# Kernel optimization log

Measured on AMD Instinct MI355X. Metric: run time of the kernel, lower is better.

## Reference

```python
import jax, jax.numpy as jnp
import numpy as np

B, S, HID, NH = 2, 2048, 2048, 16
ROPE, NOPE, VDIM = 64, 64, 128
QHEAD = ROPE + NOPE            # 128
QLORA = HID // 3               # 682
KVLORA = HID // 8              # 256
THETA = 128000.0
SCALE = 1.0 / np.sqrt(QHEAD)   # deepseek softmax_scale = q_head_dim**-0.5
EPS = 1e-6


def rmsnorm(x, w):
    var = jnp.mean(x.astype(jnp.float32) ** 2, axis=-1, keepdims=True)
    return (x.astype(jnp.float32) * jax.lax.rsqrt(var + EPS)).astype(x.dtype) * w


def rope_cos_sin(seq, dim, theta):
    inv = 1.0 / (theta ** (jnp.arange(0, dim, 2, dtype=jnp.float32) / dim))
    t = jnp.arange(seq, dtype=jnp.float32)
    freqs = jnp.outer(t, inv)                      # [S, dim/2]
    emb = jnp.concatenate([freqs, freqs], axis=-1)  # [S, dim]
    return jnp.cos(emb), jnp.sin(emb)


def apply_rope(x, cos, sin):
    # deepseek interleave: view(b,h,s,d/2,2).transpose(-1,-2).reshape, then rotate_half rope
    b, h, s, d = x.shape
    x = x.reshape(b, h, s, d // 2, 2).transpose(0, 1, 2, 4, 3).reshape(b, h, s, d)
    x1, x2 = jnp.split(x, 2, axis=-1)
    rot = jnp.concatenate([-x2, x1], axis=-1)
    return x * cos + rot * sin


def setup_inputs() -> dict:
    key = jax.random.key(0)
    ks = jax.random.split(key, 8)
    s = lambda fan_in: 1.0 / np.sqrt(fan_in)
    return {
        "x":        jax.random.normal(ks[0], (B, S, HID), jnp.float32),
        "q_a_w":    jax.random.normal(ks[1], (HID, QLORA), jnp.float32) * s(HID),
        "q_a_ln_w": jnp.ones((QLORA,), jnp.float32),
        "q_b_w":    jax.random.normal(ks[2], (QLORA, NH * QHEAD), jnp.float32) * s(QLORA),
        "kv_a_w":   jax.random.normal(ks[3], (HID, KVLORA + ROPE), jnp.float32) * s(HID),
        "kv_a_ln_w": jnp.ones((KVLORA,), jnp.float32),
        "kv_b_w":   jax.random.normal(ks[4], (KVLORA, NH * (NOPE + VDIM)), jnp.float32) * s(KVLORA),
        "o_w":      jax.random.normal(ks[5], (NH * VDIM, HID), jnp.float32) * s(NH * VDIM),
    }


def reference(x, q_a_w, q_a_ln_w, q_b_w, kv_a_w, kv_a_ln_w, kv_b_w, o_w):
    b, s, _ = x.shape
    # Q: low-rank down-proj -> RMSNorm -> up-proj
    q = rmsnorm(x @ q_a_w, q_a_ln_w) @ q_b_w               # [b,s,NH*QHEAD]
    q = q.reshape(b, s, NH, QHEAD).transpose(0, 2, 1, 3)   # [b,NH,s,QHEAD]
    q_nope, q_pe = q[..., :NOPE], q[..., NOPE:]
    # KV: compressed latent + shared rope key
    ckv_kpe = x @ kv_a_w                                   # [b,s,KVLORA+ROPE]
    ckv, k_pe = ckv_kpe[..., :KVLORA], ckv_kpe[..., KVLORA:]
    k_pe = k_pe.reshape(b, 1, s, ROPE)                     # shared across heads
    kv = rmsnorm(ckv, kv_a_ln_w) @ kv_b_w                  # [b,s,NH*(NOPE+VDIM)]
    kv = kv.reshape(b, s, NH, NOPE + VDIM).transpose(0, 2, 1, 3)
    k_nope, v = kv[..., :NOPE], kv[..., NOPE:]             # [b,NH,s,NOPE], [b,NH,s,VDIM]
    # decoupled RoPE on the rope split only
    cos, sin = rope_cos_sin(s, ROPE, THETA)
    q_pe = apply_rope(q_pe, cos, sin)
    k_pe = apply_rope(k_pe, cos, sin)
    qf = jnp.concatenate([q_nope, q_pe], axis=-1)          # [b,NH,s,QHEAD]
    kf = jnp.concatenate([k_nope, jnp.broadcast_to(k_pe, (b, NH, s, ROPE))], axis=-1)
    scores = jnp.einsum('bhqd,bhkd->bhqk', qf, kf) * SCALE
    causal = jnp.tril(jnp.ones((s, s), bool))
    scores = jnp.where(causal, scores, jnp.float32(-1e9))
    attn = jax.nn.softmax(scores.astype(jnp.float32), axis=-1).astype(qf.dtype)
    out = jnp.einsum('bhqk,bhkd->bhqd', attn, v)           # [b,NH,s,VDIM]
    out = out.transpose(0, 2, 1, 3).reshape(b, s, NH * VDIM)
    return out @ o_w                                       # [b,s,HID]
```

## Files before the change

kernel.cpp:

```cpp
#include <hip/hip_runtime.h>
#include <hip/hip_bf16.h>

typedef __attribute__((ext_vector_type(8))) short short8;
typedef __attribute__((ext_vector_type(4))) float f32x4;

using bf16 = __hip_bfloat16;

static constexpr int B_ = 2, S_ = 2048, HID_ = 2048, NH_ = 16;
static constexpr int ROPE_ = 64, VDIM_ = 128, QHEAD_ = 128;
static constexpr int QLORA_ = 682, KVLORA_ = 256;
static constexpr int QLORA_P = 704;
static constexpr int NQA_P = 768;
static constexpr int NKVA_P = 384;
static constexpr int NA_ = NQA_P + NKVA_P;
static constexpr float THETA_ = 128000.0f;
static constexpr float SCALE_ = 0.08838834764831845f;
static constexpr float SCL2_ = 0.08838834764831845f * 1.4426950408889634f;
static constexpr float EPS_ = 1e-6f;
static constexpr int BS_ = B_ * S_;

__device__ __forceinline__ void gl2lds16(const void* g, void* l) {
    __builtin_amdgcn_global_load_lds(
        (const __attribute__((address_space(1))) unsigned int*)g,
        (__attribute__((address_space(3))) unsigned int*)l, 16, 0, 0);
}

struct bf16x4_s { bf16 x, y, z, w; };

struct TD { const float* src; bf16* dst; int Ksrc, Nsrc, Kpad, tilesX, off, perm; };
struct TDs { TD d[5]; };
static constexpr int PREP_TILES = 8576;

__global__ void k_prep(TDs P, const float* __restrict__ x, bf16* __restrict__ xb,
                       float* __restrict__ ct, float* __restrict__ st) {
    __shared__ float tile[32][33];
    if (blockIdx.x >= PREP_TILES) {
        int bid = blockIdx.x - PREP_TILES;
        int t = threadIdx.y * 32 + threadIdx.x;
        if (bid < 8192) {
            int i = bid * 256 + t;
            float4 v = reinterpret_cast<const float4*>(x)[i];
            bf16x4_s o;
            o.x = __float2bfloat16(v.x); o.y = __float2bfloat16(v.y);
            o.z = __float2bfloat16(v.z); o.w = __float2bfloat16(v.w);
            reinterpret_cast<bf16x4_s*>(xb)[i] = o;
        } else {
            int idx = (bid - 8192) * 256 + t;
            int tpos = idx >> 5, j = idx & 31;
            float inv = expf(-(float)j * (logf(THETA_) / 32.0f));
            float f = (float)tpos * inv;
            ct[idx] = cosf(f);
            st[idx] = sinf(f);
        }
        return;
    }
    int flat = blockIdx.x;
    int di = 0;
    #pragma unroll
    for (int i = 1; i < 5; ++i) if (flat >= P.d[i].off) di = i;
    TD d = P.d[di];
    int local = flat - d.off;
    int xt = local % d.tilesX, yt = local / d.tilesX;
    int kb = xt * 32, nb = yt * 32;
    int tx = threadIdx.x, ty = threadIdx.y;
    #pragma unroll
    for (int i = 0; i < 32; i += 8) {
        int k = kb + ty + i, n = nb + tx;
        tile[ty + i][tx] = (k < d.Ksrc && n < d.Nsrc) ? d.src[(size_t)k * d.Nsrc + n] : 0.0f;
    }
    __syncthreads();
    #pragma unroll
    for (int i = 0; i < 32; i += 8) {
        int n = nb + ty + i, k = kb + tx;
        int nd = n;
        if (d.perm) {
            int h = n / 192, dd = n - h * 192;
            nd = (dd < 64) ? h * 64 + dd : 1024 + h * 128 + (dd - 64);
        }
        d.dst[(size_t)nd * d.Kpad + k] = __float2bfloat16(tile[tx][ty + i]);
    }
}

#define GEMM_PROLOGUE(Aptr, Bptr, LDA, LDB, KDIM)                                        \
    __shared__ bf16 As[128 * 64];                                                        \
    __shared__ bf16 Bs[128 * 64];                                                        \
    const int t = threadIdx.x;                                                           \
    const int lane = t & 63, w = t >> 6;                                                 \
    const int l15 = lane & 15, l4 = lane >> 4;                                           \
    const int wr = (w >> 1) * 64, wc = (w & 1) * 64;                                     \
    const int m0 = blockIdx.y * 128, n0 = blockIdx.x * 128;                              \
    f32x4 acc[4][4] = {};                                                                \
    for (int k0 = 0; k0 < (KDIM); k0 += 64) {                                            \
        _Pragma("unroll")                                                                \
        for (int i = 0; i < 4; ++i) {                                                    \
            int cid = t + i * 256;                                                       \
            int row = cid >> 3;                                                          \
            int ch = (cid & 7) ^ (row & 7);                                              \
            gl2lds16((Aptr) + (size_t)(m0 + row) * (LDA) + k0 + ch * 8,                  \
                     reinterpret_cast<char*>(As) + cid * 16);                            \
            gl2lds16((Bptr) + (size_t)(n0 + row) * (LDB) + k0 + ch * 8,                  \
                     reinterpret_cast<char*>(Bs) + cid * 16);                            \
        }                                                                                \
        __syncthreads();                                                                 \
        _Pragma("unroll")                                                                \
        for (int kk = 0; kk < 2; ++kk) {                                                 \
            short8 a[4], b[4];                                                           \
            _Pragma("unroll")                                                            \
            for (int m = 0; m < 4; ++m) {                                                \
                int row = wr + m * 16 + l15;                                             \
                int ch = (kk * 4 + l4) ^ (row & 7);                                      \
                a[m] = *reinterpret_cast<const short8*>(                                 \
                    reinterpret_cast<const char*>(As) + row * 128 + ch * 16);            \
            }                                                                            \
            _Pragma("unroll")                                                            \
            for (int n = 0; n < 4; ++n) {                                                \
                int row = wc + n * 16 + l15;                                             \
                int ch = (kk * 4 + l4) ^ (row & 7);                                      \
                b[n] = *reinterpret_cast<const short8*>(                                 \
                    reinterpret_cast<const char*>(Bs) + row * 128 + ch * 16);            \
            }                                                                            \
            _Pragma("unroll")                                                            \
            for (int m = 0; m < 4; ++m)                                                  \
                _Pragma("unroll")                                                        \
                for (int n = 0; n < 4; ++n)                                              \
                    acc[m][n] = __builtin_amdgcn_mfma_f32_16x16x32_bf16(a[m], b[n],      \
                                                                       acc[m][n], 0, 0, 0); \
        }                                                                                \
        __syncthreads();                                                                 \
    }

template <typename OutT>
__launch_bounds__(256)
__global__ void gemm_bt(const bf16* __restrict__ A, const bf16* __restrict__ Bt,
                        OutT* __restrict__ C, int K, int lda, int ldb, int ldc)
{
    GEMM_PROLOGUE(A, Bt, lda, ldb, K)
    #pragma unroll
    for (int m = 0; m < 4; ++m)
        #pragma unroll
        for (int n = 0; n < 4; ++n)
            #pragma unroll
            for (int j = 0; j < 4; ++j) {
                int r = m0 + wr + m * 16 + l4 * 4 + j;
                int c = n0 + wc + n * 16 + l15;
                float v = acc[m][n][j];
                if constexpr (sizeof(OutT) == 2) C[(size_t)r * ldc + c] = __float2bfloat16(v);
                else                             C[(size_t)r * ldc + c] = v;
            }
}

__launch_bounds__(256)
__global__ void gemm_qb_rope(const bf16* __restrict__ A, const bf16* __restrict__ Bt,
                             const float* __restrict__ ct, const float* __restrict__ st,
                             bf16* __restrict__ Qf)
{
    GEMM_PROLOGUE(A, Bt, QLORA_P, QLORA_P, QLORA_P)
    const int h = blockIdx.x;
    if (wc == 0) {
        #pragma unroll
        for (int m = 0; m < 4; ++m)
            #pragma unroll
            for (int n = 0; n < 4; ++n)
                #pragma unroll
                for (int j = 0; j < 4; ++j) {
                    int r = m0 + wr + m * 16 + l4 * 4 + j;
                    int c = n * 16 + l15;
                    int s = r & (S_ - 1), bq = r >> 11;
                    Qf[((size_t)(bq * NH_ + h) * S_ + s) * 128 + c] =
                        __float2bfloat16(acc[m][n][j] * SCL2_);
                }
    } else {
        #pragma unroll
        for (int m = 0; m < 4; ++m)
            #pragma unroll
            for (int n = 0; n < 4; ++n)
                #pragma unroll
                for (int j = 0; j < 4; ++j) {
                    int r = m0 + wr + m * 16 + l4 * 4 + j;
                    int p = n * 16 + l15;
                    int jj = p >> 1, odd = p & 1;
                    float v = acc[m][n][j];
                    float pr = __shfl_xor(v, 1);
                    float e0 = odd ? pr : v, e1 = odd ? v : pr;
                    int s = r & (S_ - 1), bq = r >> 11;
                    float c_ = ct[s * 32 + jj], s_ = st[s * 32 + jj];
                    float ov = odd ? (e1 * c_ + e0 * s_) : (e0 * c_ - e1 * s_);
                    int c_out = 64 + (odd ? 32 : 0) + jj;
                    Qf[((size_t)(bq * NH_ + h) * S_ + s) * 128 + c_out] =
                        __float2bfloat16(ov * SCL2_);
                }
    }
}

__launch_bounds__(256)
__global__ void gemm_kvb_split(const bf16* __restrict__ A, const bf16* __restrict__ Bt,
                               bf16* __restrict__ knope, bf16* __restrict__ Vt)
{
    GEMM_PROLOGUE(A, Bt, KVLORA_, KVLORA_, KVLORA_)
    if (n0 < 1024) {
        #pragma unroll
        for (int m = 0; m < 4; ++m)
            #pragma unroll
            for (int n = 0; n < 4; ++n)
                #pragma unroll
                for (int j = 0; j < 4; ++j) {
                    int r = m0 + wr + m * 16 + l4 * 4 + j;
                    int c = n0 + wc + n * 16 + l15;
                    knope[(size_t)r * 1024 + c] = __float2bfloat16(acc[m][n][j]);
                }
    } else {
        const int h = (n0 - 1024) >> 7;
        const int bq = m0 >> 11;
        const int bh = bq * NH_ + h;
        #pragma unroll
        for (int m = 0; m < 4; ++m)
            #pragma unroll
            for (int n = 0; n < 4; ++n) {
                int cl = wc + n * 16 + l15;
                int rb = m0 + wr + m * 16 + l4 * 4;
                int s = rb & (S_ - 1);
                ushort4 pk;
                {
                    bf16 h0 = __float2bfloat16(acc[m][n][0]);
                    bf16 h1 = __float2bfloat16(acc[m][n][1]);
                    bf16 h2 = __float2bfloat16(acc[m][n][2]);
                    bf16 h3 = __float2bfloat16(acc[m][n][3]);
                    pk.x = *reinterpret_cast<unsigned short*>(&h0);
                    pk.y = *reinterpret_cast<unsigned short*>(&h1);
                    pk.z = *reinterpret_cast<unsigned short*>(&h2);
                    pk.w = *reinterpret_cast<unsigned short*>(&h3);
                }
                *reinterpret_cast<ushort4*>(Vt + ((size_t)bh * 128 + cl) * S_ + s) = pk;
            }
    }
}

__launch_bounds__(256)
__global__ void k_rms_rope(const bf16* __restrict__ qac,
                           const float* __restrict__ qln, const float* __restrict__ kvln,
                           const float* __restrict__ ct, const float* __restrict__ st,
                           bf16* __restrict__ qan, bf16* __restrict__ ckvn, bf16* __restrict__ kr)
{
    __shared__ float red[8];
    int bs = blockIdx.x;
    int t = threadIdx.x, lane = t & 63, w = t >> 6;
    int s = bs & (S_ - 1);
    const bf16* qrow = qac + (size_t)bs * NA_;
    const bf16* crow = qrow + NQA_P;
    float sq = 0.f, sk;
    for (int c = t; c < QLORA_; c += 256) { float v = __bfloat162float(qrow[c]); sq += v * v; }
    { float v = __bfloat162float(crow[t]); sk = v * v; }
    #pragma unroll
    for (int m = 1; m < 64; m <<= 1) { sq += __shfl_xor(sq, m); sk += __shfl_xor(sk, m); }
    if (lane == 0) { red[w] = sq; red[4 + w] = sk; }
    __syncthreads();
    sq = red[0] + red[1] + red[2] + red[3];
    sk = red[4] + red[5] + red[6] + red[7];
    float qs = rsqrtf(sq / (float)QLORA_ + EPS_);
    float ks = rsqrtf(sk / (float)KVLORA_ + EPS_);
    for (int c = t; c < QLORA_P; c += 256)
        qan[(size_t)bs * QLORA_P + c] =
            (c < QLORA_) ? __float2bfloat16(__bfloat162float(qrow[c]) * qs * qln[c])
                         : __float2bfloat16(0.0f);
    ckvn[(size_t)bs * KVLORA_ + t] = __float2bfloat16(__bfloat162float(crow[t]) * ks * kvln[t]);
    if (t < 64) {
        int j = t & 31;
        float c_ = ct[s * 32 + j], s_ = st[s * 32 + j];
        float e0 = __bfloat162float(crow[KVLORA_ + 2 * j]);
        float e1 = __bfloat162float(crow[KVLORA_ + 2 * j + 1]);
        float v = (t < 32) ? (e0 * c_ - e1 * s_) : (e1 * c_ + e0 * s_);
        kr[(size_t)bs * 64 + t] = __float2bfloat16(v);
    }
}

__launch_bounds__(512, 4)
__global__ void k_flash(const bf16* __restrict__ Qf, const bf16* __restrict__ knope,
                        const bf16* __restrict__ kr, const bf16* __restrict__ Vt,
                        bf16* __restrict__ attn_out)
{
    __shared__ bf16 Ks[2][64 * 128];
    __shared__ bf16 Vs[2][128 * 64];
    __shared__ bf16 Ps[8][16 * 64];

    const int t = threadIdx.x, lane = t & 63, w = t >> 6;
    const int l15 = lane & 15, l4 = lane >> 4;
    const int qb = (blockIdx.y < 8) ? (15 - blockIdx.y) : (blockIdx.y - 8);
    const int bh = blockIdx.x;
    const int q0 = qb * 128;
    const int b = bh >> 4, h = bh & 15;
    const int r0 = q0 + w * 16;

    short8 qa_[4];
    {
        const bf16* qrow = Qf + ((size_t)bh * S_ + r0 + l15) * 128;
        #pragma unroll
        for (int kk = 0; kk < 4; ++kk)
            qa_[kk] = *reinterpret_cast<const short8*>(qrow + kk * 32 + l4 * 8);
    }

    const bf16 *kSrc0, *kSrc1, *vSrc0, *vSrc1;
    size_t kStp0, kStp1;
    {
        int cid = t, row = cid >> 4, ch = (cid & 15) ^ (row & 7);
        kSrc0 = (ch < 8) ? knope + (size_t)(b * S_ + row) * 1024 + h * 64 + ch * 8
                         : kr + (size_t)(b * S_ + row) * 64 + (ch - 8) * 8;
        kStp0 = (ch < 8) ? (size_t)64 * 1024 : (size_t)64 * 64;
    }
    {
        int cid = t + 512, row = cid >> 4, ch = (cid & 15) ^ (row & 7);
        kSrc1 = (ch < 8) ? knope + (size_t)(b * S_ + row) * 1024 + h * 64 + ch * 8
                         : kr + (size_t)(b * S_ + row) * 64 + (ch - 8) * 8;
        kStp1 = (ch < 8) ? (size_t)64 * 1024 : (size_t)64 * 64;
    }
    {
        const bf16* Vg = Vt + (size_t)bh * 128 * S_;
        int cid = t, row = cid >> 3, ch = (cid & 7) ^ (row & 7);
        vSrc0 = Vg + (size_t)row * S_ + ch * 8;
        cid = t + 512; row = cid >> 3; ch = (cid & 7) ^ (row & 7);
        vSrc1 = Vg + (size_t)row * S_ + ch * 8;
    }
    auto stage = [&](int buf) {
        gl2lds16(kSrc0, reinterpret_cast<char*>(Ks[buf]) + t * 16);
        gl2lds16(kSrc1, reinterpret_cast<char*>(Ks[buf]) + (t + 512) * 16);
        gl2lds16(vSrc0, reinterpret_cast<char*>(Vs[buf]) + t * 16);
        gl2lds16(vSrc1, reinterpret_cast<char*>(Vs[buf]) + (t + 512) * 16);
        kSrc0 += kStp0; kSrc1 += kStp1; vSrc0 += 64; vSrc1 += 64;
    };

    const int NT = qb * 2 + 2;
    stage(0);
    __syncthreads();

    f32x4 o[8] = {};
    float m_r[4], l_r[4];
    #pragma unroll
    for (int j = 0; j < 4; ++j) { m_r[j] = -1e30f; l_r[j] = 0.f; }

    int cur = 0;
    for (int kb = 0; kb < NT; ++kb) {
        const int k0 = kb * 64;
        if (kb + 1 < NT) stage(cur ^ 1);

        if (k0 <= r0 + 15) {
            f32x4 sfr[4] = {};
            __builtin_amdgcn_s_setprio(1);
            #pragma unroll
            for (int kk = 0; kk < 4; ++kk) {
                short8 bfr[4];
                #pragma unroll
                for (int n = 0; n < 4; ++n) {
                    int row = n * 16 + l15;
                    int ch = (kk * 4 + l4) ^ (row & 7);
                    bfr[n] = *reinterpret_cast<const short8*>(
                        reinterpret_cast<const char*>(Ks[cur]) + row * 256 + ch * 16);
                }
                #pragma unroll
                for (int n = 0; n < 4; ++n)
                    sfr[n] = __builtin_amdgcn_mfma_f32_16x16x32_bf16(qa_[kk], bfr[n], sfr[n], 0, 0, 0);
            }
            __builtin_amdgcn_s_setprio(0);

            const bool needMask = (k0 + 63 > r0);
            if (needMask) {
                #pragma unroll
                for (int n = 0; n < 4; ++n)
                    #pragma unroll
                    for (int j = 0; j < 4; ++j) {
                        int col = k0 + n * 16 + l15;
                        int row = r0 + l4 * 4 + j;
                        if (col > row) sfr[n][j] = -1e30f;
                    }
            }

            float rm[4];
            bool grow = false;
            #pragma unroll
            for (int j = 0; j < 4; ++j) {
                float r = fmaxf(fmaxf(sfr[0][j], sfr[1][j]), fmaxf(sfr[2][j], sfr[3][j]));
                r = fmaxf(r, __shfl_xor(r, 1));
                r = fmaxf(r, __shfl_xor(r, 2));
                r = fmaxf(r, __shfl_xor(r, 4));
                r = fmaxf(r, __shfl_xor(r, 8));
                rm[j] = r;
                grow |= (r > m_r[j] + 8.0f);
            }
            if (__ballot(grow)) {
                #pragma unroll
                for (int j = 0; j < 4; ++j) {
                    float mn = fmaxf(m_r[j], rm[j]);
                    float alpha = exp2f(m_r[j] - mn);
                    m_r[j] = mn;
                    l_r[j] *= alpha;
                    #pragma unroll
                    for (int n = 0; n < 8; ++n) o[n][j] *= alpha;
                }
            }

            char* pb = reinterpret_cast<char*>(Ps[w]);
            #pragma unroll
            for (int j = 0; j < 4; ++j) {
                float rs = 0.f;
                #pragma unroll
                for (int n = 0; n < 4; ++n) {
                    float p = exp2f(sfr[n][j] - m_r[j]);
                    sfr[n][j] = p;
                    rs += p;
                }
                rs += __shfl_xor(rs, 1); rs += __shfl_xor(rs, 2);
                rs += __shfl_xor(rs, 4); rs += __shfl_xor(rs, 8);
                l_r[j] += rs;
                int row = l4 * 4 + j;
                #pragma unroll
                for (int n = 0; n < 4; ++n) {
                    int col = n * 16 + l15;
                    int ch = (col >> 3) ^ (row & 7);
                    *reinterpret_cast<bf16*>(pb + row * 128 + ch * 16 + (col & 7) * 2) =
                        __float2bfloat16(sfr[n][j]);
                }
            }
            __builtin_amdgcn_s_setprio(1);
            #pragma unroll
            for (int kk = 0; kk < 2; ++kk) {
                int pch = (kk * 4 + l4) ^ (l15 & 7);
                short8 pa = *reinterpret_cast<const short8*>(pb + l15 * 128 + pch * 16);
                #pragma unroll
                for (int n = 0; n < 8; ++n) {
                    int row = n * 16 + l15;
                    int ch = (kk * 4 + l4) ^ (row & 7);
                    short8 vb = *reinterpret_cast<const short8*>(
                        reinterpret_cast<const char*>(Vs[cur]) + row * 128 + ch * 16);
                    o[n] = __builtin_amdgcn_mfma_f32_16x16x32_bf16(pa, vb, o[n], 0, 0, 0);
                }
            }
            __builtin_amdgcn_s_setprio(0);
        }
        __syncthreads();
        cur ^= 1;
    }

    size_t obase = ((size_t)(b * S_) + q0 + w * 16) * (size_t)(NH_ * VDIM_) + h * VDIM_;
    #pragma unroll
    for (int n = 0; n < 8; ++n)
        #pragma unroll
        for (int j = 0; j < 4; ++j) {
            int r = l4 * 4 + j;
            int c = n * 16 + l15;
            attn_out[obase + (size_t)r * (NH_ * VDIM_) + c] = __float2bfloat16(o[n][j] / l_r[j]);
        }
}

extern "C" void kernel_launch(void* const* d_in, const int* in_sizes, int n_in,
                              void* d_out, int out_size, void* d_ws, size_t ws_size,
                              hipStream_t stream)
{
    (void)in_sizes; (void)n_in; (void)out_size;
    const float* x       = (const float*)d_in[0];
    const float* q_a_w   = (const float*)d_in[1];
    const float* q_a_ln  = (const float*)d_in[2];
    const float* q_b_w   = (const float*)d_in[3];
    const float* kv_a_w  = (const float*)d_in[4];
    const float* kv_a_ln = (const float*)d_in[5];
    const float* kv_b_w  = (const float*)d_in[6];
    const float* o_w     = (const float*)d_in[7];
    float* out = (float*)d_out;

    char* ws = (char*)d_ws;
    size_t off = 0;
    auto alloc = [&](size_t bytes) -> char* {
        char* p = ws + off;
        off += (bytes + 255) & ~(size_t)255;
        return p;
    };

    bf16* xb     = (bf16*)alloc((size_t)BS_ * HID_ * 2);
    bf16* a_wt   = (bf16*)alloc((size_t)NA_ * HID_ * 2);
    bf16* qb_wt  = (bf16*)alloc((size_t)2048 * QLORA_P * 2);
    bf16* kvb_wt = (bf16*)alloc((size_t)3072 * KVLORA_ * 2);
    bf16* ow_t   = (bf16*)alloc((size_t)2048 * 2048 * 2);
    float* ct    = (float*)alloc((size_t)S_ * 32 * 4);
    float* st    = (float*)alloc((size_t)S_ * 32 * 4);
    bf16* qac    = (bf16*)alloc((size_t)BS_ * NA_ * 2);
    bf16* qan    = (bf16*)alloc((size_t)BS_ * QLORA_P * 2);
    bf16* ckvn   = (bf16*)alloc((size_t)BS_ * KVLORA_ * 2);
    bf16* kr     = (bf16*)alloc((size_t)BS_ * 64 * 2);
    bf16* knope  = (bf16*)alloc((size_t)BS_ * 1024 * 2);
    bf16* Vt     = (bf16*)alloc((size_t)BS_ * 2048 * 2);
    bf16* attn   = (bf16*)alloc((size_t)BS_ * 2048 * 2);

    bf16* Qf = xb;

    if (ws_size < off) return;

    TDs P;
    P.d[0] = TD{ q_a_w,  a_wt,                      2048,  682, 2048, 64,    0, 0 };
    P.d[1] = TD{ kv_a_w, a_wt + (size_t)NQA_P*2048, 2048,  320, 2048, 64, 1536, 0 };
    P.d[2] = TD{ q_b_w,  qb_wt,                      682, 2048,  704, 22, 2304, 0 };
    P.d[3] = TD{ kv_b_w, kvb_wt,                     256, 3072,  256,  8, 3712, 1 };
    P.d[4] = TD{ o_w,    ow_t,                      2048, 2048, 2048, 64, 4480, 0 };
    k_prep<<<PREP_TILES + 8192 + 256, dim3(32, 8), 0, stream>>>(P, x, xb, ct, st);

    gemm_bt<bf16><<<dim3(NA_ / 128, BS_ / 128), 256, 0, stream>>>(xb, a_wt, qac,
                                                                  HID_, HID_, HID_, NA_);

    k_rms_rope<<<BS_, 256, 0, stream>>>(qac, q_a_ln, kv_a_ln, ct, st, qan, ckvn, kr);

    gemm_qb_rope<<<dim3(2048 / 128, BS_ / 128), 256, 0, stream>>>(qan, qb_wt, ct, st, Qf);
    gemm_kvb_split<<<dim3(3072 / 128, BS_ / 128), 256, 0, stream>>>(ckvn, kvb_wt, knope, Vt);

    k_flash<<<dim3(B_ * NH_, S_ / 128), 512, 0, stream>>>(Qf, knope, kr, Vt, attn);

    gemm_bt<float><<<dim3(2048 / 128, BS_ / 128), 256, 0, stream>>>(attn, ow_t, out,
                                                                    HID_, HID_, HID_, 2048);
}
```

Baseline: 264.8 us.

## Merge Q/KV up-projection GEMMs into one launch and transpose flash S tile

Fuses the q_b+rope GEMM and the kv_b split GEMM into a single kernel whose grid is partitioned by blockIdx.x, removing a launch and letting both GEMMs share the device at once. In the flash kernel the QK^T MFMA operands are swapped so each lane holds scores for a single query row. This turns per-row max/sum reductions into two cross-lane shuffles instead of four per row for four rows, and lets P be written as packed bf16x4 stores. Rescale factors are now broadcast by shuffle, which adds some shuffle work on rescale and at the final normalization.

```diff
diff --git a/kernel.cpp b/kernel.cpp
--- a/kernel.cpp
+++ b/kernel.cpp
@@ -81,14 +81,16 @@
     }
 }
 
-#define GEMM_PROLOGUE(Aptr, Bptr, LDA, LDB, KDIM)                                        \
+#define GEMM_VARS                                                                        \
     __shared__ bf16 As[128 * 64];                                                        \
     __shared__ bf16 Bs[128 * 64];                                                        \
     const int t = threadIdx.x;                                                           \
     const int lane = t & 63, w = t >> 6;                                                 \
     const int l15 = lane & 15, l4 = lane >> 4;                                           \
-    const int wr = (w >> 1) * 64, wc = (w & 1) * 64;                                     \
-    const int m0 = blockIdx.y * 128, n0 = blockIdx.x * 128;                              \
+    const int wr = (w >> 1) * 64, wc = (w & 1) * 64;
+
+#define GEMM_CORE(Aptr, Bptr, LDA, LDB, KDIM, M0V, N0V)                                  \
+    const int m0 = (M0V), n0 = (N0V);                                                    \
     f32x4 acc[4][4] = {};                                                                \
     for (int k0 = 0; k0 < (KDIM); k0 += 64) {                                            \
         _Pragma("unroll")                                                                \
@@ -134,7 +136,8 @@
 __global__ void gemm_bt(const bf16* __restrict__ A, const bf16* __restrict__ Bt,
                         OutT* __restrict__ C, int K, int lda, int ldb, int ldc)
 {
-    GEMM_PROLOGUE(A, Bt, lda, ldb, K)
+    GEMM_VARS
+    GEMM_CORE(A, Bt, lda, ldb, K, blockIdx.y * 128, blockIdx.x * 128)
     #pragma unroll
     for (int m = 0; m < 4; ++m)
         #pragma unroll
@@ -150,88 +153,90 @@
 }
 
 __launch_bounds__(256)
-__global__ void gemm_qb_rope(const bf16* __restrict__ A, const bf16* __restrict__ Bt,
-                             const float* __restrict__ ct, const float* __restrict__ st,
-                             bf16* __restrict__ Qf)
+__global__ void gemm_up(const bf16* __restrict__ qan, const bf16* __restrict__ qb_wt,
+                        const float* __restrict__ ct, const float* __restrict__ st,
+                        bf16* __restrict__ Qf,
+                        const bf16* __restrict__ ckvn, const bf16* __restrict__ kvb_wt,
+                        bf16* __restrict__ knope, bf16* __restrict__ Vt)
 {
-    GEMM_PROLOGUE(A, Bt, QLORA_P, QLORA_P, QLORA_P)
-    const int h = blockIdx.x;
-    if (wc == 0) {
-        #pragma unroll
-        for (int m = 0; m < 4; ++m)
-            #pragma unroll
-            for (int n = 0; n < 4; ++n)
-                #pragma unroll
-                for (int j = 0; j < 4; ++j) {
-                    int r = m0 + wr + m * 16 + l4 * 4 + j;
-                    int c = n * 16 + l15;
-                    int s = r & (S_ - 1), bq = r >> 11;
-                    Qf[((size_t)(bq * NH_ + h) * S_ + s) * 128 + c] =
-                        __float2bfloat16(acc[m][n][j] * SCL2_);
+    GEMM_VARS
+    if (blockIdx.x < 16) {
+        GEMM_CORE(qan, qb_wt, QLORA_P, QLORA_P, QLORA_P, blockIdx.y * 128, blockIdx.x * 128)
+        (void)n0;
+        const int h = blockIdx.x;
+        if (wc == 0) {
+            #pragma unroll
+            for (int m = 0; m < 4; ++m)
+                #pragma unroll
+                for (int n = 0; n < 4; ++n)
+                    #pragma unroll
+                    for (int j = 0; j < 4; ++j) {
+                        int r = m0 + wr + m * 16 + l4 * 4 + j;
+                        int c = n * 16 + l15;
+                        int s = r & (S_ - 1), bq = r >> 11;
+                        Qf[((size_t)(bq * NH_ + h) * S_ + s) * 128 + c] =
+                            __float2bfloat16(acc[m][n][j] * SCL2_);
+                    }
+        } else {
+            #pragma unroll
+            for (int m = 0; m < 4; ++m)
+                #pragma unroll
+                for (int n = 0; n < 4; ++n)
+                    #pragma unroll
+                    for (int j = 0; j < 4; ++j) {
+                        int r = m0 + wr + m * 16 + l4 * 4 + j;
+                        int p = n * 16 + l15;
+                        int jj = p >> 1, odd = p & 1;
+                        float v = acc[m][n][j];
+                        float pr = __shfl_xor(v, 1);
+                        float e0 = odd ? pr : v, e1 = odd ? v : pr;
+                        int s = r & (S_ - 1), bq = r >> 11;
+                        float c_ = ct[s * 32 + jj], s_ = st[s * 32 + jj];
+                        float ov = odd ? (e1 * c_ + e0 * s_) : (e0 * c_ - e1 * s_);
+                        int c_out = 64 + (odd ? 32 : 0) + jj;
+                        Qf[((size_t)(bq * NH_ + h) * S_ + s) * 128 + c_out] =
+                            __float2bfloat16(ov * SCL2_);
+                    }
+        }
+    } else {
+        GEMM_CORE(ckvn, kvb_wt, KVLORA_, KVLORA_, KVLORA_, blockIdx.y * 128,
+                  (blockIdx.x - 16) * 128)
+        if (n0 < 1024) {
+            #pragma unroll
+            for (int m = 0; m < 4; ++m)
+                #pragma unroll
+                for (int n = 0; n < 4; ++n)
+                    #pragma unroll
+                    for (int j = 0; j < 4; ++j) {
+                        int r = m0 + wr + m * 16 + l4 * 4 + j;
+                        int c = n0 + wc + n * 16 + l15;
+                        knope[(size_t)r * 1024 + c] = __float2bfloat16(acc[m][n][j]);
+                    }
+        } else {
+            const int h = (n0 - 1024) >> 7;
+            const int bq = m0 >> 11;
+            const int bh = bq * NH_ + h;
+            #pragma unroll
+            for (int m = 0; m < 4; ++m)
+                #pragma unroll
+                for (int n = 0; n < 4; ++n) {
+                    int cl = wc + n * 16 + l15;
+                    int rb = m0 + wr + m * 16 + l4 * 4;
+                    int s = rb & (S_ - 1);
+                    ushort4 pk;
+                    {
+                        bf16 h0 = __float2bfloat16(acc[m][n][0]);
+                        bf16 h1 = __float2bfloat16(acc[m][n][1]);
+                        bf16 h2 = __float2bfloat16(acc[m][n][2]);
+                        bf16 h3 = __float2bfloat16(acc[m][n][3]);
+                        pk.x = *reinterpret_cast<unsigned short*>(&h0);
+                        pk.y = *reinterpret_cast<unsigned short*>(&h1);
+                        pk.z = *reinterpret_cast<unsigned short*>(&h2);
+                        pk.w = *reinterpret_cast<unsigned short*>(&h3);
+                    }
+                    *reinterpret_cast<ushort4*>(Vt + ((size_t)bh * 128 + cl) * S_ + s) = pk;
                 }
-    } else {
-        #pragma unroll
-        for (int m = 0; m < 4; ++m)
-            #pragma unroll
-            for (int n = 0; n < 4; ++n)
-                #pragma unroll
-                for (int j = 0; j < 4; ++j) {
-                    int r = m0 + wr + m * 16 + l4 * 4 + j;
-                    int p = n * 16 + l15;
-                    int jj = p >> 1, odd = p & 1;
-                    float v = acc[m][n][j];
-                    float pr = __shfl_xor(v, 1);
-                    float e0 = odd ? pr : v, e1 = odd ? v : pr;
-                    int s = r & (S_ - 1), bq = r >> 11;
-                    float c_ = ct[s * 32 + jj], s_ = st[s * 32 + jj];
-                    float ov = odd ? (e1 * c_ + e0 * s_) : (e0 * c_ - e1 * s_);
-                    int c_out = 64 + (odd ? 32 : 0) + jj;
-                    Qf[((size_t)(bq * NH_ + h) * S_ + s) * 128 + c_out] =
-                        __float2bfloat16(ov * SCL2_);
-                }
-    }
-}
-
-__launch_bounds__(256)
-__global__ void gemm_kvb_split(const bf16* __restrict__ A, const bf16* __restrict__ Bt,
-                               bf16* __restrict__ knope, bf16* __restrict__ Vt)
-{
-    GEMM_PROLOGUE(A, Bt, KVLORA_, KVLORA_, KVLORA_)
-    if (n0 < 1024) {
-        #pragma unroll
-        for (int m = 0; m < 4; ++m)
-            #pragma unroll
-            for (int n = 0; n < 4; ++n)
-                #pragma unroll
-                for (int j = 0; j < 4; ++j) {
-                    int r = m0 + wr + m * 16 + l4 * 4 + j;
-                    int c = n0 + wc + n * 16 + l15;
-                    knope[(size_t)r * 1024 + c] = __float2bfloat16(acc[m][n][j]);
-                }
-    } else {
-        const int h = (n0 - 1024) >> 7;
-        const int bq = m0 >> 11;
-        const int bh = bq * NH_ + h;
-        #pragma unroll
-        for (int m = 0; m < 4; ++m)
-            #pragma unroll
-            for (int n = 0; n < 4; ++n) {
-                int cl = wc + n * 16 + l15;
-                int rb = m0 + wr + m * 16 + l4 * 4;
-                int s = rb & (S_ - 1);
-                ushort4 pk;
-                {
-                    bf16 h0 = __float2bfloat16(acc[m][n][0]);
-                    bf16 h1 = __float2bfloat16(acc[m][n][1]);
-                    bf16 h2 = __float2bfloat16(acc[m][n][2]);
-                    bf16 h3 = __float2bfloat16(acc[m][n][3]);
-                    pk.x = *reinterpret_cast<unsigned short*>(&h0);
-                    pk.y = *reinterpret_cast<unsigned short*>(&h1);
-                    pk.z = *reinterpret_cast<unsigned short*>(&h2);
-                    pk.w = *reinterpret_cast<unsigned short*>(&h3);
-                }
-                *reinterpret_cast<ushort4*>(Vt + ((size_t)bh * 128 + cl) * S_ + s) = pk;
-            }
+        }
     }
 }
 
@@ -332,9 +337,7 @@
     __syncthreads();
 
     f32x4 o[8] = {};
-    float m_r[4], l_r[4];
-    #pragma unroll
-    for (int j = 0; j < 4; ++j) { m_r[j] = -1e30f; l_r[j] = 0.f; }
+    float m_r = -1e30f, l_r = 0.f;
 
     int cur = 0;
     for (int kb = 0; kb < NT; ++kb) {
@@ -346,78 +349,77 @@
             __builtin_amdgcn_s_setprio(1);
             #pragma unroll
             for (int kk = 0; kk < 4; ++kk) {
-                short8 bfr[4];
-                #pragma unroll
-                for (int n = 0; n < 4; ++n) {
-                    int row = n * 16 + l15;
+                short8 kf[4];
+                #pragma unroll
+                for (int m = 0; m < 4; ++m) {
+                    int row = m * 16 + l15;
                     int ch = (kk * 4 + l4) ^ (row & 7);
-                    bfr[n] = *reinterpret_cast<const short8*>(
+                    kf[m] = *reinterpret_cast<const short8*>(
                         reinterpret_cast<const char*>(Ks[cur]) + row * 256 + ch * 16);
                 }
                 #pragma unroll
-                for (int n = 0; n < 4; ++n)
-                    sfr[n] = __builtin_amdgcn_mfma_f32_16x16x32_bf16(qa_[kk], bfr[n], sfr[n], 0, 0, 0);
+                for (int m = 0; m < 4; ++m)
+                    sfr[m] = __builtin_amdgcn_mfma_f32_16x16x32_bf16(kf[m], qa_[kk], sfr[m], 0, 0, 0);
             }
             __builtin_amdgcn_s_setprio(0);
 
-            const bool needMask = (k0 + 63 > r0);
-            if (needMask) {
-                #pragma unroll
-                for (int n = 0; n < 4; ++n)
+            const int qrow = r0 + l15;
+            if (k0 + 63 > r0) {
+                #pragma unroll
+                for (int m = 0; m < 4; ++m) {
+                    int kbase = k0 + m * 16 + l4 * 4;
                     #pragma unroll
-                    for (int j = 0; j < 4; ++j) {
-                        int col = k0 + n * 16 + l15;
-                        int row = r0 + l4 * 4 + j;
-                        if (col > row) sfr[n][j] = -1e30f;
-                    }
-            }
-
-            float rm[4];
-            bool grow = false;
-            #pragma unroll
-            for (int j = 0; j < 4; ++j) {
-                float r = fmaxf(fmaxf(sfr[0][j], sfr[1][j]), fmaxf(sfr[2][j], sfr[3][j]));
-                r = fmaxf(r, __shfl_xor(r, 1));
-                r = fmaxf(r, __shfl_xor(r, 2));
-                r = fmaxf(r, __shfl_xor(r, 4));
-                r = fmaxf(r, __shfl_xor(r, 8));
-                rm[j] = r;
-                grow |= (r > m_r[j] + 8.0f);
-            }
-            if (__ballot(grow)) {
-                #pragma unroll
-                for (int j = 0; j < 4; ++j) {
-                    float mn = fmaxf(m_r[j], rm[j]);
-                    float alpha = exp2f(m_r[j] - mn);
-                    m_r[j] = mn;
-                    l_r[j] *= alpha;
+                    for (int j = 0; j < 4; ++j)
+                        if (kbase + j > qrow) sfr[m][j] = -1e30f;
+                }
+            }
+
+            float rm;
+            {
+                float a0 = fmaxf(fmaxf(sfr[0][0], sfr[0][1]), fmaxf(sfr[0][2], sfr[0][3]));
+                float a1 = fmaxf(fmaxf(sfr[1][0], sfr[1][1]), fmaxf(sfr[1][2], sfr[1][3]));
+                float a2 = fmaxf(fmaxf(sfr[2][0], sfr[2][1]), fmaxf(sfr[2][2], sfr[2][3]));
+                float a3 = fmaxf(fmaxf(sfr[3][0], sfr[3][1]), fmaxf(sfr[3][2], sfr[3][3]));
+                rm = fmaxf(fmaxf(a0, a1), fmaxf(a2, a3));
+            }
+            rm = fmaxf(rm, __shfl_xor(rm, 16));
+            rm = fmaxf(rm, __shfl_xor(rm, 32));
+
+            if (__ballot(rm > m_r + 8.0f)) {
+                float mn = fmaxf(m_r, rm);
+                float alpha = exp2f(m_r - mn);
+                m_r = mn;
+                l_r *= alpha;
+                float aj[4];
+                #pragma unroll
+                for (int j = 0; j < 4; ++j) aj[j] = __shfl(alpha, l4 * 4 + j);
+                #pragma unroll
+                for (int n = 0; n < 8; ++n)
                     #pragma unroll
-                    for (int n = 0; n < 8; ++n) o[n][j] *= alpha;
-                }
+                    for (int j = 0; j < 4; ++j) o[n][j] *= aj[j];
             }
 
             char* pb = reinterpret_cast<char*>(Ps[w]);
-            #pragma unroll
-            for (int j = 0; j < 4; ++j) {
-                float rs = 0.f;
-                #pragma unroll
-                for (int n = 0; n < 4; ++n) {
-                    float p = exp2f(sfr[n][j] - m_r[j]);
-                    sfr[n][j] = p;
-                    rs += p;
-                }
-                rs += __shfl_xor(rs, 1); rs += __shfl_xor(rs, 2);
-                rs += __shfl_xor(rs, 4); rs += __shfl_xor(rs, 8);
-                l_r[j] += rs;
-                int row = l4 * 4 + j;
-                #pragma unroll
-                for (int n = 0; n < 4; ++n) {
-                    int col = n * 16 + l15;
-                    int ch = (col >> 3) ^ (row & 7);
-                    *reinterpret_cast<bf16*>(pb + row * 128 + ch * 16 + (col & 7) * 2) =
-                        __float2bfloat16(sfr[n][j]);
-                }
-            }
+            float rs = 0.f;
+            #pragma unroll
+            for (int m = 0; m < 4; ++m) {
+                float p0 = exp2f(sfr[m][0] - m_r);
+                float p1 = exp2f(sfr[m][1] - m_r);
+                float p2 = exp2f(sfr[m][2] - m_r);
+                float p3 = exp2f(sfr[m][3] - m_r);
+                rs += (p0 + p1) + (p2 + p3);
+                union { __hip_bfloat162 h; unsigned int u; } cl, ch2;
+                cl.h  = __float22bfloat162_rn(make_float2(p0, p1));
+                ch2.h = __float22bfloat162_rn(make_float2(p2, p3));
+                int kloc = m * 16 + l4 * 4;
+                int chnk = (kloc >> 3) ^ (l15 & 7);
+                uint2 pk2; pk2.x = cl.u; pk2.y = ch2.u;
+                *reinterpret_cast<uint2*>(pb + l15 * 128 + chnk * 16 + (kloc & 7) * 2) = pk2;
+            }
+            rs += __shfl_xor(rs, 16);
+            rs += __shfl_xor(rs, 32);
+            l_r += rs;
+
             __builtin_amdgcn_s_setprio(1);
             #pragma unroll
             for (int kk = 0; kk < 2; ++kk) {
@@ -438,6 +440,9 @@
         cur ^= 1;
     }
 
+    float lj[4];
+    #pragma unroll
+    for (int j = 0; j < 4; ++j) lj[j] = __shfl(l_r, l4 * 4 + j);
     size_t obase = ((size_t)(b * S_) + q0 + w * 16) * (size_t)(NH_ * VDIM_) + h * VDIM_;
     #pragma unroll
     for (int n = 0; n < 8; ++n)
@@ -445,7 +450,7 @@
         for (int j = 0; j < 4; ++j) {
             int r = l4 * 4 + j;
             int c = n * 16 + l15;
-            attn_out[obase + (size_t)r * (NH_ * VDIM_) + c] = __float2bfloat16(o[n][j] / l_r[j]);
+            attn_out[obase + (size_t)r * (NH_ * VDIM_) + c] = __float2bfloat16(o[n][j] / lj[j]);
         }
 }
 
@@ -504,8 +509,8 @@
 
     k_rms_rope<<<BS_, 256, 0, stream>>>(qac, q_a_ln, kv_a_ln, ct, st, qan, ckvn, kr);
 
-    gemm_qb_rope<<<dim3(2048 / 128, BS_ / 128), 256, 0, stream>>>(qan, qb_wt, ct, st, Qf);
-    gemm_kvb_split<<<dim3(3072 / 128, BS_ / 128), 256, 0, stream>>>(ckvn, kvb_wt, knope, Vt);
+    gemm_up<<<dim3(16 + 24, BS_ / 128), 256, 0, stream>>>(qan, qb_wt, ct, st, Qf,
+                                                          ckvn, kvb_wt, knope, Vt);
 
     k_flash<<<dim3(B_ * NH_, S_ / 128), 512, 0, stream>>>(Qf, knope, kr, Vt, attn);
 
```

Result: faster. 229.5 us (-13.3%).
